# Kernel optimization log

Hardware: AMD Instinct MI355X
Metric: run time of the kernel (lower is better)

The kernel has to match this reference:

```python
import jax, jax.numpy as jnp
import numpy as np

NUM_REAL = 19          # real classes (ignore class = index 19 is excluded by cls_counts[:, :-1])
MAX_FEATS_TOTAL = 10000
TEMPERATURE = 0.5
EPS_NORM = 1e-12       # torch F.normalize eps


def setup_inputs() -> dict:
    key = jax.random.key(0)
    k1, k2 = jax.random.split(key)
    label = jax.random.randint(k1, (4, 1024, 1024), 0, NUM_REAL, dtype=jnp.int32)
    features = jax.random.normal(k2, (4, 256, 256, 256), dtype=jnp.float32)
    return {"label": label, "features": features}


def _forward(label, features):
    n, c, fh, fw = features.shape
    scale = label.shape[-1] // fw
    # get_dist_and_classes: nearest-neighbour downsample == strided slice (exact divisor)
    dom = label[:, ::scale, ::scale].reshape(n, -1)               # [N, P]
    P = dom.shape[1]
    feats = features.reshape(n, c, P)                             # [N, C, P]

    # sample_anchors_fast: all NUM_REAL classes present in every image (guaranteed by setup),
    # so total_cls and views_per_class are static (the max_features_total cap path).
    T = n * NUM_REAL
    V = MAX_FEATS_TOTAL // T

    mask = dom[:, None, :] == jnp.arange(NUM_REAL, dtype=dom.dtype)[None, :, None]  # [N,K,P]
    pix = jnp.arange(P, dtype=jnp.int32)
    # key > 0 iff pixel belongs to class; larger key = earlier pixel -> top_k picks the
    # first V member pixels per (image, class) (deterministic stand-in for randperm)
    sel_key = jnp.where(mask, P - pix, -pix)
    _, idx = jax.lax.top_k(sel_key, V)                            # [N, K, V]

    sampled = jnp.take_along_axis(feats[:, None, :, :], idx[:, :, None, :], axis=3)  # [N,K,C,V]
    sampled = sampled.reshape(T, c, V)                            # batch-major, class ascending
    labels = jnp.tile(jnp.arange(NUM_REAL, dtype=jnp.float32), n) # [T]

    # contrastive_loss
    norm = jnp.sqrt(jnp.sum(sampled * sampled, axis=1, keepdims=True))
    f = sampled / jnp.maximum(norm, EPS_NORM)                     # L2 normalize over C
    f = jnp.transpose(f, (0, 2, 1)).reshape(T * V, c)             # [T*V, C]
    lab = jnp.repeat(labels, V)                                   # [T*V]

    eq = (lab[:, None] == lab[None, :]).astype(f.dtype)           # [TV, TV]
    M = T * V
    d = jnp.arange(M)
    pos_mask = eq.at[d, d].set(0.0)

    logits = (f @ f.T) / TEMPERATURE
    exp_l = jnp.exp(logits)                                       # original has no max-subtraction
    neg_sum = jnp.sum(exp_l * (1.0 - eq), axis=1, keepdims=True)
    log_prob = logits - jnp.log(exp_l + neg_sum)
    mean_log_prob_pos = jnp.sum(pos_mask * log_prob, axis=1) / jnp.sum(pos_mask, axis=1)
    return -jnp.mean(mean_log_prob_pos)


def reference(label, features):
    return _forward(label, features)
```

## Files before the change

kernel.cpp:

```cpp
#include <hip/hip_runtime.h>
#include <hip/hip_bf16.h>

#define NUM_REAL 19
#define NIMG     4
#define T_TOT    76
#define V_SEL    131
#define M_ROWS   9956
#define MP       9984
#define CDIM     256
#define P_PIX    65536
#define TILE     128
#define BK       32
#define RPI      2489
#define NT1      3081
#define NCHUNK   32
#define CHPIX    2048
#define CT       5
#define NT2      (NUM_REAL * 15)

typedef __attribute__((ext_vector_type(8))) short short8;
typedef __attribute__((ext_vector_type(4))) float floatx4;

__device__ __forceinline__ void gld_lds16(const unsigned short* g, unsigned short* l) {
    __builtin_amdgcn_global_load_lds((__attribute__((address_space(1))) void*)(g),
                                     (__attribute__((address_space(3))) void*)(l),
                                     16, 0, 0);
}

__global__ __launch_bounds__(256) void k_hist(const int* __restrict__ label,
                                              int* __restrict__ ghist)
{
    __shared__ int h[NUM_REAL];
    const int img = blockIdx.y, ch = blockIdx.x, tid = threadIdx.x;
    if (tid < NUM_REAL) h[tid] = 0;
    __syncthreads();
    const int* lab = label + img * 1048576;
    const int p0 = ch * CHPIX + tid * 8;
    #pragma unroll
    for (int j = 0; j < 8; ++j) {
        int p = p0 + j;
        int c = lab[((p >> 8) << 12) + ((p & 255) << 2)];
        atomicAdd(&h[c], 1);
    }
    __syncthreads();
    if (tid < NUM_REAL) ghist[(img * NCHUNK + ch) * NUM_REAL + tid] = h[tid];
}

__global__ __launch_bounds__(256) void k_scatter(const int* __restrict__ label,
                                                 const int* __restrict__ ghist,
                                                 int* __restrict__ sel)
{
    __shared__ int cnt[NUM_REAL * 256];
    const int img = blockIdx.y, ch = blockIdx.x, tid = threadIdx.x;
    #pragma unroll
    for (int k = 0; k < NUM_REAL; ++k) cnt[k * 256 + tid] = 0;
    __shared__ int base[NUM_REAL];
    if (tid < NUM_REAL) {
        int b = 0;
        for (int q = 0; q < ch; ++q) b += ghist[(img * NCHUNK + q) * NUM_REAL + tid];
        base[tid] = b;
    }
    const int* lab = label + img * 1048576;
    const int p0 = ch * CHPIX + tid * 8;
    #pragma unroll
    for (int j = 0; j < 8; ++j) {
        int p = p0 + j;
        int c = lab[((p >> 8) << 12) + ((p & 255) << 2)];
        cnt[c * 256 + tid]++;
    }
    __syncthreads();
    if (tid < NUM_REAL) {
        int run = base[tid], bb = tid * 256;
        for (int t2 = 0; t2 < 256; ++t2) {
            int tmp = cnt[bb + t2];
            cnt[bb + t2] = run;
            run += tmp;
        }
    }
    __syncthreads();
    bool need = false;
    #pragma unroll
    for (int k = 0; k < NUM_REAL; ++k) if (cnt[k * 256 + tid] < V_SEL) need = true;
    if (need) {
        for (int j = 0; j < 8; ++j) {
            int p = p0 + j;
            int c = lab[((p >> 8) << 12) + ((p & 255) << 2)];
            int r = cnt[c * 256 + tid]++;
            if (r < V_SEL) sel[(img * NUM_REAL + c) * V_SEL + r] = p;
        }
    }
}

__global__ __launch_bounds__(256) void k_gather1(const float* __restrict__ feats,
                                                 const int* __restrict__ sel,
                                                 float* __restrict__ Ftmp,
                                                 float* __restrict__ nrm)
{
    __shared__ int pbuf[RPI];
    const int b  = blockIdx.y;
    const int c0 = blockIdx.x * 4;
    const int tid = threadIdx.x;
    for (int s = tid; s < RPI; s += 256) pbuf[s] = sel[b * RPI + s];
    __syncthreads();
    const float* f0 = feats + (size_t)(b * CDIM + c0) * P_PIX;
    for (int r = tid; r < RPI; r += 256) {
        int p = pbuf[r];
        float x0 = f0[p];
        float x1 = f0[p + P_PIX];
        float x2 = f0[p + 2 * P_PIX];
        float x3 = f0[p + 3 * P_PIX];
        int row = b * RPI + r;
        float4 v = make_float4(x0, x1, x2, x3);
        *reinterpret_cast<float4*>(Ftmp + (size_t)row * CDIM + c0) = v;
        atomicAdd(&nrm[row], x0 * x0 + x1 * x1 + x2 * x2 + x3 * x3);
    }
}

__global__ __launch_bounds__(256) void k_gather2(const float* __restrict__ Ftmp,
                                                 const float* __restrict__ nrm,
                                                 unsigned short* __restrict__ F)
{
    const int row = blockIdx.x * 4 + (threadIdx.x >> 6);
    const int c4  = (threadIdx.x & 63) * 4;
    ushort4 o;
    if (row < M_ROWS) {
        float4 v = *reinterpret_cast<const float4*>(Ftmp + (size_t)row * CDIM + c4);
        float rinv = 1.0f / fmaxf(sqrtf(nrm[row]), 1e-12f);
        __hip_bfloat16 h0 = __float2bfloat16(v.x * rinv);
        __hip_bfloat16 h1 = __float2bfloat16(v.y * rinv);
        __hip_bfloat16 h2 = __float2bfloat16(v.z * rinv);
        __hip_bfloat16 h3 = __float2bfloat16(v.w * rinv);
        o.x = *reinterpret_cast<unsigned short*>(&h0);
        o.y = *reinterpret_cast<unsigned short*>(&h1);
        o.z = *reinterpret_cast<unsigned short*>(&h2);
        o.w = *reinterpret_cast<unsigned short*>(&h3);
    } else {
        o.x = o.y = o.z = o.w = 0;
    }
    *reinterpret_cast<ushort4*>(F + (size_t)row * CDIM + c4) = o;
}

__global__ __launch_bounds__(256) void k_gemm(const unsigned short* __restrict__ F,
                                              float* __restrict__ negsum)
{
    __shared__ unsigned short As[2][TILE * BK];
    __shared__ unsigned short Bs[2][TILE * BK];

    int t = blockIdx.x;
    int bi = (int)((157.0f - sqrtf(24649.0f - 8.0f * (float)t)) * 0.5f);
    if (bi < 0) bi = 0;
    if (bi > 77) bi = 77;
    while ((bi + 1) * 78 - ((bi + 1) * bi) / 2 <= t) ++bi;
    while (bi * 78 - (bi * (bi - 1)) / 2 > t) --bi;
    int bj = bi + (t - (bi * 78 - (bi * (bi - 1)) / 2));
    const bool diag = (bi == bj);
    const int i0 = bi * TILE, j0 = bj * TILE;

    const int tid  = threadIdx.x;
    const int wave = tid >> 6, lane = tid & 63;
    const int qr = lane >> 4, lr = lane & 15;
    const int wr = (wave >> 1) * 64, wc = (wave & 1) * 64;

    floatx4 acc[4][4];
    floatx4 zero4 = {0.f, 0.f, 0.f, 0.f};
    #pragma unroll
    for (int a = 0; a < 4; ++a)
        #pragma unroll
        for (int b = 0; b < 4; ++b) acc[a][b] = zero4;

    const int srow = wave * 32 + (lane >> 2);
    const int scol = (lane & 3) * 8;
    const unsigned short* gA = F + (size_t)(i0 + srow) * CDIM + scol;
    const unsigned short* gB = F + (size_t)(j0 + srow) * CDIM + scol;
    const int l0 = (wave * 32) * BK, l1 = (wave * 32 + 16) * BK;

    gld_lds16(gA,             &As[0][l0]);
    gld_lds16(gA + 16 * CDIM, &As[0][l1]);
    gld_lds16(gB,             &Bs[0][l0]);
    gld_lds16(gB + 16 * CDIM, &Bs[0][l1]);

    #pragma unroll 2
    for (int k = 0; k < 8; ++k) {
        __syncthreads();
        const int cur = k & 1, nxt = cur ^ 1;
        if (k < 7) {
            const int kc = (k + 1) * BK;
            gld_lds16(gA + kc,             &As[nxt][l0]);
            gld_lds16(gA + kc + 16 * CDIM, &As[nxt][l1]);
            gld_lds16(gB + kc,             &Bs[nxt][l0]);
            gld_lds16(gB + kc + 16 * CDIM, &Bs[nxt][l1]);
        }
        short8 a[4], b[4];
        #pragma unroll
        for (int mi = 0; mi < 4; ++mi)
            a[mi] = *reinterpret_cast<const short8*>(&As[cur][(wr + mi * 16 + lr) * BK + qr * 8]);
        #pragma unroll
        for (int ni = 0; ni < 4; ++ni)
            b[ni] = *reinterpret_cast<const short8*>(&Bs[cur][(wc + ni * 16 + lr) * BK + qr * 8]);
        #pragma unroll
        for (int mi = 0; mi < 4; ++mi)
            #pragma unroll
            for (int ni = 0; ni < 4; ++ni)
                acc[mi][ni] = __builtin_amdgcn_mfma_f32_16x16x32_bf16(a[mi], b[ni], acc[mi][ni], 0, 0, 0);
    }

    int jcls[4];
    bool jval[4];
    #pragma unroll
    for (int ni = 0; ni < 4; ++ni) {
        int gcol = j0 + wc + ni * 16 + lr;
        jval[ni] = gcol < M_ROWS;
        unsigned tj = (unsigned)gcol / V_SEL;
        jcls[ni] = (int)(tj - (tj / NUM_REAL) * NUM_REAL);
    }
    float* red  = (float*)&As[0][0];
    float* cred = (float*)&Bs[0][0];
    float colacc[4] = {0.f, 0.f, 0.f, 0.f};
    #pragma unroll
    for (int mi = 0; mi < 4; ++mi) {
        #pragma unroll
        for (int reg = 0; reg < 4; ++reg) {
            int rloc = wr + mi * 16 + qr * 4 + reg;
            int grow = i0 + rloc;
            bool ival = grow < M_ROWS;
            unsigned ti = (unsigned)grow / V_SEL;
            int icls = (int)(ti - (ti / NUM_REAL) * NUM_REAL);
            float rowacc = 0.f;
            #pragma unroll
            for (int ni = 0; ni < 4; ++ni) {
                bool v = ival && jval[ni] && (icls != jcls[ni]);
                float e = v ? __expf(acc[mi][ni][reg] * 2.0f) : 0.f;
                rowacc += e;
                colacc[ni] += e;
            }
            rowacc += __shfl_xor(rowacc, 1, 64);
            rowacc += __shfl_xor(rowacc, 2, 64);
            rowacc += __shfl_xor(rowacc, 4, 64);
            rowacc += __shfl_xor(rowacc, 8, 64);
            if (lr == 0) red[rloc * 2 + (wave & 1)] = rowacc;
        }
    }
    #pragma unroll
    for (int ni = 0; ni < 4; ++ni) {
        float cc = colacc[ni];
        cc += __shfl_xor(cc, 16, 64);
        cc += __shfl_xor(cc, 32, 64);
        if (qr == 0) cred[(wc + ni * 16 + lr) * 2 + (wave >> 1)] = cc;
    }
    __syncthreads();
    if (tid < 128) {
        int row = i0 + tid;
        if (row < M_ROWS) atomicAdd(&negsum[row], red[tid * 2] + red[tid * 2 + 1]);
    } else {
        int cc2 = tid - 128, col = j0 + cc2;
        if (!diag && col < M_ROWS) atomicAdd(&negsum[col], cred[cc2 * 2] + cred[cc2 * 2 + 1]);
    }
}

__global__ __launch_bounds__(256) void k_pos(const unsigned short* __restrict__ F,
                                             const float* __restrict__ negsum,
                                             float* __restrict__ out)
{
    __shared__ unsigned short As[2][TILE * BK];
    __shared__ unsigned short Bs[2][TILE * BK];
    __shared__ float wred[4];

    const int c = blockIdx.x / 15;
    int pidx = blockIdx.x % 15;
    int ti = 0;
    while (pidx >= CT - ti) { pidx -= CT - ti; ++ti; }
    const int tj = ti + pidx;
    const int u0i = ti * TILE, u0j = tj * TILE;
    const bool offd = (ti != tj);

    const int tid  = threadIdx.x;
    const int wave = tid >> 6, lane = tid & 63;
    const int qr = lane >> 4, lr = lane & 15;
    const int wr = (wave >> 1) * 64, wc = (wave & 1) * 64;

    floatx4 acc[4][4];
    floatx4 zero4 = {0.f, 0.f, 0.f, 0.f};
    #pragma unroll
    for (int a = 0; a < 4; ++a)
        #pragma unroll
        for (int b = 0; b < 4; ++b) acc[a][b] = zero4;

    const int srow = wave * 32 + (lane >> 2);
    const int scol = (lane & 3) * 8;
    auto growmap = [&](int u) -> int {
        int uc = u < 524 ? u : 523;
        int b = uc / 131, v = uc - 131 * b;
        return b * RPI + c * V_SEL + v;
    };
    const unsigned short* gA0 = F + (size_t)growmap(u0i + srow) * CDIM + scol;
    const unsigned short* gA1 = F + (size_t)growmap(u0i + srow + 16) * CDIM + scol;
    const unsigned short* gB0 = F + (size_t)growmap(u0j + srow) * CDIM + scol;
    const unsigned short* gB1 = F + (size_t)growmap(u0j + srow + 16) * CDIM + scol;
    const int l0 = (wave * 32) * BK, l1 = (wave * 32 + 16) * BK;

    gld_lds16(gA0, &As[0][l0]);
    gld_lds16(gA1, &As[0][l1]);
    gld_lds16(gB0, &Bs[0][l0]);
    gld_lds16(gB1, &Bs[0][l1]);

    #pragma unroll 2
    for (int k = 0; k < 8; ++k) {
        __syncthreads();
        const int cur = k & 1, nxt = cur ^ 1;
        if (k < 7) {
            const int kc = (k + 1) * BK;
            gld_lds16(gA0 + kc, &As[nxt][l0]);
            gld_lds16(gA1 + kc, &As[nxt][l1]);
            gld_lds16(gB0 + kc, &Bs[nxt][l0]);
            gld_lds16(gB1 + kc, &Bs[nxt][l1]);
        }
        short8 a[4], b[4];
        #pragma unroll
        for (int mi = 0; mi < 4; ++mi)
            a[mi] = *reinterpret_cast<const short8*>(&As[cur][(wr + mi * 16 + lr) * BK + qr * 8]);
        #pragma unroll
        for (int ni = 0; ni < 4; ++ni)
            b[ni] = *reinterpret_cast<const short8*>(&Bs[cur][(wc + ni * 16 + lr) * BK + qr * 8]);
        #pragma unroll
        for (int mi = 0; mi < 4; ++mi)
            #pragma unroll
            for (int ni = 0; ni < 4; ++ni)
                acc[mi][ni] = __builtin_amdgcn_mfma_f32_16x16x32_bf16(a[mi], b[ni], acc[mi][ni], 0, 0, 0);
    }

    int  ujv[4];
    bool jval[4];
    float nsj[4];
    #pragma unroll
    for (int ni = 0; ni < 4; ++ni) {
        int uj = u0j + wc + ni * 16 + lr;
        ujv[ni] = uj;
        jval[ni] = uj < 524;
        nsj[ni] = jval[ni] ? negsum[growmap(uj)] : 0.f;
    }
    float tsum = 0.f;
    #pragma unroll
    for (int mi = 0; mi < 4; ++mi) {
        #pragma unroll
        for (int reg = 0; reg < 4; ++reg) {
            int ui = u0i + wr + mi * 16 + qr * 4 + reg;
            bool ival = ui < 524;
            float nsi = ival ? negsum[growmap(ui)] : 0.f;
            #pragma unroll
            for (int ni = 0; ni < 4; ++ni) {
                if (ival && jval[ni] && ui != ujv[ni]) {
                    float l  = acc[mi][ni][reg] * 2.0f;
                    float el = __expf(l);
                    tsum += l - __logf(el + nsi);
                    if (offd) tsum += l - __logf(el + nsj[ni]);
                }
            }
        }
    }
    #pragma unroll
    for (int s = 32; s > 0; s >>= 1) tsum += __shfl_xor(tsum, s, 64);
    if (lane == 0) wred[wave] = tsum;
    __syncthreads();
    if (tid == 0) {
        const float scale = -1.0f / (523.0f * (float)M_ROWS);
        atomicAdd(out, (wred[0] + wred[1] + wred[2] + wred[3]) * scale);
    }
}

extern "C" void kernel_launch(void* const* d_in, const int* in_sizes, int n_in,
                              void* d_out, int out_size, void* d_ws, size_t ws_size,
                              hipStream_t stream)
{
    const int*   label = (const int*)d_in[0];
    const float* feats = (const float*)d_in[1];
    float*       out   = (float*)d_out;

    char* ws = (char*)d_ws;
    unsigned short* F = (unsigned short*)ws;
    size_t off = (size_t)MP * CDIM * 2;
    int* sel = (int*)(ws + off);
    off += (size_t)T_TOT * V_SEL * 4;
    off = (off + 255) & ~(size_t)255;
    float* negsum = (float*)(ws + off);
    off += (size_t)MP * 4;
    float* nrm = (float*)(ws + off);
    off += (size_t)MP * 4;
    int* ghist = (int*)(ws + off);
    off += (size_t)NIMG * NCHUNK * NUM_REAL * 4;
    off = (off + 255) & ~(size_t)255;
    float* Ftmp = (float*)(ws + off);

    hipMemsetAsync(negsum, 0, (size_t)MP * 8, stream);
    hipMemsetAsync(out, 0, sizeof(float), stream);

    dim3 gh(NCHUNK, NIMG);
    k_hist<<<gh, 256, 0, stream>>>(label, ghist);
    k_scatter<<<gh, 256, 0, stream>>>(label, ghist, sel);
    dim3 g1(CDIM / 4, NIMG);
    k_gather1<<<g1, 256, 0, stream>>>(feats, sel, Ftmp, nrm);
    k_gather2<<<MP / 4, 256, 0, stream>>>(Ftmp, nrm, F);
    k_gemm<<<NT1, 256, 0, stream>>>(F, negsum);
    k_pos<<<NT2, 256, 0, stream>>>(F, negsum, out);
}
```

Before: 433.3 us.

## Load GEMM operands directly from global into registers, rotate gather row order

The GEMM and positive-pair kernels no longer stage bf16 tiles through LDS with global_load_lds and per-step barriers. Each wave now loads its MFMA fragments straight from global memory into double-buffered registers, which removes LDS traffic and __syncthreads. The trade-off is that operand reuse moves from LDS to L1/L2, raising global load traffic and register pressure. The gather kernel also rotates its starting row chunk per block to spread concurrent accesses to the same rows.

```diff
diff --git a/kernel.cpp b/kernel.cpp
--- a/kernel.cpp
+++ b/kernel.cpp
@@ -21,12 +21,6 @@
 typedef __attribute__((ext_vector_type(8))) short short8;
 typedef __attribute__((ext_vector_type(4))) float floatx4;
 
-__device__ __forceinline__ void gld_lds16(const unsigned short* g, unsigned short* l) {
-    __builtin_amdgcn_global_load_lds((__attribute__((address_space(1))) void*)(g),
-                                     (__attribute__((address_space(3))) void*)(l),
-                                     16, 0, 0);
-}
-
 __global__ __launch_bounds__(256) void k_hist(const int* __restrict__ label,
                                               int* __restrict__ ghist)
 {
@@ -103,7 +97,11 @@
     for (int s = tid; s < RPI; s += 256) pbuf[s] = sel[b * RPI + s];
     __syncthreads();
     const float* f0 = feats + (size_t)(b * CDIM + c0) * P_PIX;
-    for (int r = tid; r < RPI; r += 256) {
+    const int NIT = (RPI + 255) / 256;
+    const int rot = blockIdx.x % NIT;
+    for (int s = 0; s < NIT; ++s) {
+        int r = ((s + rot) % NIT) * 256 + tid;
+        if (r >= RPI) continue;
         int p = pbuf[r];
         float x0 = f0[p];
         float x1 = f0[p + P_PIX];
@@ -143,8 +141,8 @@
 __global__ __launch_bounds__(256) void k_gemm(const unsigned short* __restrict__ F,
                                               float* __restrict__ negsum)
 {
-    __shared__ unsigned short As[2][TILE * BK];
-    __shared__ unsigned short Bs[2][TILE * BK];
+    __shared__ float red[TILE * 2];
+    __shared__ float cred[TILE * 2];
 
     int t = blockIdx.x;
     int bi = (int)((157.0f - sqrtf(24649.0f - 8.0f * (float)t)) * 0.5f);
@@ -168,40 +166,29 @@
         #pragma unroll
         for (int b = 0; b < 4; ++b) acc[a][b] = zero4;
 
-    const int srow = wave * 32 + (lane >> 2);
-    const int scol = (lane & 3) * 8;
-    const unsigned short* gA = F + (size_t)(i0 + srow) * CDIM + scol;
-    const unsigned short* gB = F + (size_t)(j0 + srow) * CDIM + scol;
-    const int l0 = (wave * 32) * BK, l1 = (wave * 32 + 16) * BK;
-
-    gld_lds16(gA,             &As[0][l0]);
-    gld_lds16(gA + 16 * CDIM, &As[0][l1]);
-    gld_lds16(gB,             &Bs[0][l0]);
-    gld_lds16(gB + 16 * CDIM, &Bs[0][l1]);
-
-    #pragma unroll 2
+    const short8* pA = reinterpret_cast<const short8*>(F + (size_t)(i0 + wr + lr) * CDIM) + qr;
+    const short8* pB = reinterpret_cast<const short8*>(F + (size_t)(j0 + wc + lr) * CDIM) + qr;
+
+    short8 a[2][4], b[2][4];
+    #pragma unroll
+    for (int mi = 0; mi < 4; ++mi) a[0][mi] = pA[mi * 512];
+    #pragma unroll
+    for (int ni = 0; ni < 4; ++ni) b[0][ni] = pB[ni * 512];
+
+    #pragma unroll
     for (int k = 0; k < 8; ++k) {
-        __syncthreads();
         const int cur = k & 1, nxt = cur ^ 1;
         if (k < 7) {
-            const int kc = (k + 1) * BK;
-            gld_lds16(gA + kc,             &As[nxt][l0]);
-            gld_lds16(gA + kc + 16 * CDIM, &As[nxt][l1]);
-            gld_lds16(gB + kc,             &Bs[nxt][l0]);
-            gld_lds16(gB + kc + 16 * CDIM, &Bs[nxt][l1]);
-        }
-        short8 a[4], b[4];
+            #pragma unroll
+            for (int mi = 0; mi < 4; ++mi) a[nxt][mi] = pA[mi * 512 + (k + 1) * 4];
+            #pragma unroll
+            for (int ni = 0; ni < 4; ++ni) b[nxt][ni] = pB[ni * 512 + (k + 1) * 4];
+        }
         #pragma unroll
         for (int mi = 0; mi < 4; ++mi)
-            a[mi] = *reinterpret_cast<const short8*>(&As[cur][(wr + mi * 16 + lr) * BK + qr * 8]);
-        #pragma unroll
-        for (int ni = 0; ni < 4; ++ni)
-            b[ni] = *reinterpret_cast<const short8*>(&Bs[cur][(wc + ni * 16 + lr) * BK + qr * 8]);
-        #pragma unroll
-        for (int mi = 0; mi < 4; ++mi)
             #pragma unroll
             for (int ni = 0; ni < 4; ++ni)
-                acc[mi][ni] = __builtin_amdgcn_mfma_f32_16x16x32_bf16(a[mi], b[ni], acc[mi][ni], 0, 0, 0);
+                acc[mi][ni] = __builtin_amdgcn_mfma_f32_16x16x32_bf16(a[cur][mi], b[cur][ni], acc[mi][ni], 0, 0, 0);
     }
 
     int jcls[4];
@@ -213,8 +200,6 @@
         unsigned tj = (unsigned)gcol / V_SEL;
         jcls[ni] = (int)(tj - (tj / NUM_REAL) * NUM_REAL);
     }
-    float* red  = (float*)&As[0][0];
-    float* cred = (float*)&Bs[0][0];
     float colacc[4] = {0.f, 0.f, 0.f, 0.f};
     #pragma unroll
     for (int mi = 0; mi < 4; ++mi) {
@@ -261,8 +246,6 @@
                                              const float* __restrict__ negsum,
                                              float* __restrict__ out)
 {
-    __shared__ unsigned short As[2][TILE * BK];
-    __shared__ unsigned short Bs[2][TILE * BK];
     __shared__ float wred[4];
 
     const int c = blockIdx.x / 15;
@@ -285,47 +268,40 @@
         #pragma unroll
         for (int b = 0; b < 4; ++b) acc[a][b] = zero4;
 
-    const int srow = wave * 32 + (lane >> 2);
-    const int scol = (lane & 3) * 8;
     auto growmap = [&](int u) -> int {
         int uc = u < 524 ? u : 523;
         int b = uc / 131, v = uc - 131 * b;
         return b * RPI + c * V_SEL + v;
     };
-    const unsigned short* gA0 = F + (size_t)growmap(u0i + srow) * CDIM + scol;
-    const unsigned short* gA1 = F + (size_t)growmap(u0i + srow + 16) * CDIM + scol;
-    const unsigned short* gB0 = F + (size_t)growmap(u0j + srow) * CDIM + scol;
-    const unsigned short* gB1 = F + (size_t)growmap(u0j + srow + 16) * CDIM + scol;
-    const int l0 = (wave * 32) * BK, l1 = (wave * 32 + 16) * BK;
-
-    gld_lds16(gA0, &As[0][l0]);
-    gld_lds16(gA1, &As[0][l1]);
-    gld_lds16(gB0, &Bs[0][l0]);
-    gld_lds16(gB1, &Bs[0][l1]);
-
-    #pragma unroll 2
+    const short8* pAm[4];
+    const short8* pBn[4];
+    #pragma unroll
+    for (int mi = 0; mi < 4; ++mi)
+        pAm[mi] = reinterpret_cast<const short8*>(F + (size_t)growmap(u0i + wr + mi * 16 + lr) * CDIM) + qr;
+    #pragma unroll
+    for (int ni = 0; ni < 4; ++ni)
+        pBn[ni] = reinterpret_cast<const short8*>(F + (size_t)growmap(u0j + wc + ni * 16 + lr) * CDIM) + qr;
+
+    short8 a[2][4], b[2][4];
+    #pragma unroll
+    for (int mi = 0; mi < 4; ++mi) a[0][mi] = pAm[mi][0];
+    #pragma unroll
+    for (int ni = 0; ni < 4; ++ni) b[0][ni] = pBn[ni][0];
+
+    #pragma unroll
     for (int k = 0; k < 8; ++k) {
-        __syncthreads();
         const int cur = k & 1, nxt = cur ^ 1;
         if (k < 7) {
-            const int kc = (k + 1) * BK;
-            gld_lds16(gA0 + kc, &As[nxt][l0]);
-            gld_lds16(gA1 + kc, &As[nxt][l1]);
-            gld_lds16(gB0 + kc, &Bs[nxt][l0]);
-            gld_lds16(gB1 + kc, &Bs[nxt][l1]);
-        }
-        short8 a[4], b[4];
+            #pragma unroll
+            for (int mi = 0; mi < 4; ++mi) a[nxt][mi] = pAm[mi][(k + 1) * 4];
+            #pragma unroll
+            for (int ni = 0; ni < 4; ++ni) b[nxt][ni] = pBn[ni][(k + 1) * 4];
+        }
         #pragma unroll
         for (int mi = 0; mi < 4; ++mi)
-            a[mi] = *reinterpret_cast<const short8*>(&As[cur][(wr + mi * 16 + lr) * BK + qr * 8]);
-        #pragma unroll
-        for (int ni = 0; ni < 4; ++ni)
-            b[ni] = *reinterpret_cast<const short8*>(&Bs[cur][(wc + ni * 16 + lr) * BK + qr * 8]);
-        #pragma unroll
-        for (int mi = 0; mi < 4; ++mi)
             #pragma unroll
             for (int ni = 0; ni < 4; ++ni)
-                acc[mi][ni] = __builtin_amdgcn_mfma_f32_16x16x32_bf16(a[mi], b[ni], acc[mi][ni], 0, 0, 0);
+                acc[mi][ni] = __builtin_amdgcn_mfma_f32_16x16x32_bf16(a[cur][mi], b[cur][ni], acc[mi][ni], 0, 0, 0);
     }
 
     int  ujv[4];
```

Result: slower. 486.6 us (+12.3%).
